# Kernel tuning notes

Measured on AMD Instinct MI355X. Metric: run time of the kernel, lower is better.

The kernel has to match this reference:

```python
import jax, jax.numpy as jnp
import numpy as np

B, TM1, ENC, DEC, OUT = 256, 32, 128, 128, 1


def setup_inputs() -> dict:
    key = jax.random.key(0)
    ks = jax.random.split(key, 16)
    s = 0.05
    inp = {
        "input_encoded": jax.random.normal(ks[0], (B, TM1, ENC), jnp.float32),
        "y_history": jax.random.normal(ks[1], (B, TM1, OUT), jnp.float32),
        # attn_layer: Linear(2*DEC+ENC -> ENC), Tanh, Linear(ENC -> 1)
        "attn_W1": jax.random.normal(ks[2], (ENC, 2 * DEC + ENC), jnp.float32) * s,
        "attn_b1": jnp.zeros((ENC,), jnp.float32),
        "attn_W2": jax.random.normal(ks[3], (1, ENC), jnp.float32) * s,
        "attn_b2": jnp.zeros((1,), jnp.float32),
        # LSTM(input_size=OUT, hidden_size=DEC), pytorch gate order i,f,g,o
        "W_ih": jax.random.normal(ks[4], (4 * DEC, OUT), jnp.float32) * s,
        "W_hh": jax.random.normal(ks[5], (4 * DEC, DEC), jnp.float32) * s,
        "b_ih": jnp.zeros((4 * DEC,), jnp.float32),
        "b_hh": jnp.zeros((4 * DEC,), jnp.float32),
        # fc: Linear(ENC+OUT -> OUT), weight initialized with normal_() in torch
        "fc_W": jax.random.normal(ks[6], (OUT, ENC + OUT), jnp.float32),
        "fc_b": jnp.zeros((OUT,), jnp.float32),
        # fc_final: Linear(DEC+ENC -> OUT)
        "fcf_W": jax.random.normal(ks[7], (OUT, DEC + ENC), jnp.float32) * s,
        "fcf_b": jnp.zeros((OUT,), jnp.float32),
    }
    return inp


def _forward(input_encoded, y_history, attn_W1, attn_b1, attn_W2, attn_b2,
             W_ih, W_hh, b_ih, b_hh, fc_W, fc_b, fcf_W, fcf_b):
    b, tm1, enc = input_encoded.shape
    dec = W_hh.shape[1]

    h0 = jnp.zeros((b, dec), input_encoded.dtype)
    c0 = jnp.zeros((b, dec), input_encoded.dtype)
    ctx0 = jnp.zeros((b, enc), input_encoded.dtype)

    def step(carry, y_t):  # y_t: [B, OUT]
        h, c, _ = carry
        hc = jnp.concatenate([h, c], axis=-1)  # [B, 2*DEC]
        x = jnp.concatenate(
            [jnp.broadcast_to(hc[:, None, :], (b, tm1, 2 * dec)), input_encoded],
            axis=-1)  # [B, T-1, 2*DEC+ENC]
        hdn = jnp.tanh(jnp.einsum('bte,he->bth', x, attn_W1) + attn_b1)
        logits = jnp.einsum('bth,oh->bto', hdn, attn_W2)[..., 0] + attn_b2[0]  # [B, T-1]
        attn = jax.nn.softmax(logits, axis=1)
        ctx = jnp.einsum('bt,bte->be', attn, input_encoded)  # [B, ENC]
        y_tilde = jnp.concatenate([ctx, y_t], axis=1) @ fc_W.T + fc_b  # [B, OUT]
        gates = y_tilde @ W_ih.T + b_ih + h @ W_hh.T + b_hh  # [B, 4*DEC]
        i, f, g, o = jnp.split(gates, 4, axis=-1)
        c_new = jax.nn.sigmoid(f) * c + jax.nn.sigmoid(i) * jnp.tanh(g)
        h_new = jax.nn.sigmoid(o) * jnp.tanh(c_new)
        return (h_new, c_new, ctx), None

    (h, c, ctx), _ = jax.lax.scan(step, (h0, c0, ctx0),
                                  jnp.swapaxes(y_history, 0, 1))
    out = jnp.concatenate([h, ctx], axis=1) @ fcf_W.T + fcf_b + y_history[:, -1]
    return out  # [B, OUT]


def reference(input_encoded, y_history, attn_W1, attn_b1, attn_W2, attn_b2,
              W_ih, W_hh, b_ih, b_hh, fc_W, fc_b, fcf_W, fcf_b):
    return _forward(input_encoded, y_history, attn_W1, attn_b1, attn_W2, attn_b2,
                    W_ih, W_hh, b_ih, b_hh, fc_W, fc_b, fcf_W, fcf_b)
```

## Files before the change

### kernel.cpp

```cpp
#include <hip/hip_runtime.h>


#define TT 32

typedef _Float16 h2_t __attribute__((ext_vector_type(2)));
typedef _Float16 h4_t __attribute__((ext_vector_type(4)));
typedef _Float16 h8_t __attribute__((ext_vector_type(8)));

#if __has_builtin(__builtin_amdgcn_fdot2)
#define FDOT2(a, b, c) __builtin_amdgcn_fdot2((a), (b), (c), false)
#else
static __device__ __forceinline__ float FDOT2(h2_t a, h2_t b, float c) {
    return c + (float)a[0] * (float)b[0] + (float)a[1] * (float)b[1];
}
#endif

__device__ __forceinline__ float dot_h8(h8_t w, h8_t v, float acc) {
    acc = FDOT2(__builtin_shufflevector(w, w, 0, 1), __builtin_shufflevector(v, v, 0, 1), acc);
    acc = FDOT2(__builtin_shufflevector(w, w, 2, 3), __builtin_shufflevector(v, v, 2, 3), acc);
    acc = FDOT2(__builtin_shufflevector(w, w, 4, 5), __builtin_shufflevector(v, v, 4, 5), acc);
    acc = FDOT2(__builtin_shufflevector(w, w, 6, 7), __builtin_shufflevector(v, v, 6, 7), acc);
    return acc;
}
__device__ __forceinline__ h8_t pk8(float4 a, float4 b) {
    h8_t r;
    r[0] = (_Float16)a.x; r[1] = (_Float16)a.y; r[2] = (_Float16)a.z; r[3] = (_Float16)a.w;
    r[4] = (_Float16)b.x; r[5] = (_Float16)b.y; r[6] = (_Float16)b.z; r[7] = (_Float16)b.w;
    return r;
}
__device__ __forceinline__ float fast_tanh(float x) {
    float e = __expf(2.f * x);
    return 1.f - __fdividef(2.f, e + 1.f);
}
__device__ __forceinline__ float fast_sig(float x) {
    return __fdividef(1.f, 1.f + __expf(-x));
}

__global__ __launch_bounds__(512, 2) void decoder_kernel(
    const float* __restrict__ enc_g,
    const float* __restrict__ yh_g,
    const float* __restrict__ W1,
    const float* __restrict__ b1,
    const float* __restrict__ W2,
    const float* __restrict__ b2,
    const float* __restrict__ Wih,
    const float* __restrict__ Whh,
    const float* __restrict__ bih,
    const float* __restrict__ bhh,
    const float* __restrict__ fcW,
    const float* __restrict__ fcB,
    const float* __restrict__ fcfW,
    const float* __restrict__ fcfB,
    float* __restrict__ out)
{
    __shared__ __align__(16) h8_t s_w1a8[512 * 8];
    __shared__ __align__(16) _Float16 s_enc16[TT * 136];
    __shared__ __align__(16) _Float16 s_epre16[TT * 128];
    __shared__ __align__(16) _Float16 s_hc[2 * 272];
    __shared__ __align__(16) _Float16 s_A16[128];
    __shared__ __align__(16) _Float16 s_w216[128];
    __shared__ __align__(16) float s_act[512];
    __shared__ float s_logit[TT];
    __shared__ float s_q[TT];
    __shared__ float s_att[TT];
    __shared__ float s_yh[TT];
    __shared__ float s_ctx[128];

    const int tid = threadIdx.x;
    const int b = blockIdx.x;
    const int lane = tid & 63;
    const int g1 = tid >> 2, s4 = tid & 3;
    const int rx7 = tid & 7;

    {
        const float4* encp = (const float4*)(enc_g + (size_t)b * TT * 128);
#pragma unroll
        for (int r = 0; r < 2; r++) {
            int gi = tid * 2 + r;
            float4 v = encp[gi];
            int t = gi >> 5, e4 = gi & 31;
            h4_t hv;
            hv[0] = (_Float16)v.x; hv[1] = (_Float16)v.y;
            hv[2] = (_Float16)v.z; hv[3] = (_Float16)v.w;
            *(h4_t*)(s_enc16 + t * 136 + e4 * 4) = hv;
        }
    }
    if (tid < 272) ((unsigned int*)s_hc)[tid] = 0u;
    if (tid < 128) s_w216[tid] = (_Float16)W2[tid];
    if (tid < TT) s_yh[tid] = yh_g[b * TT + tid];

    h8_t whhreg[16];
    {
        const float4* wp = (const float4*)(Whh + (size_t)tid * 128);
#pragma unroll
        for (int k = 0; k < 16; k++) whhreg[k] = pk8(wp[2 * k], wp[2 * k + 1]);
    }
    const float wih_r = Wih[tid];
    const float bias_r = bih[tid] + bhh[tid];

    {
        const float4* p = (const float4*)(W1 + g1 * 384 + s4 * 64);
#pragma unroll
        for (int k = 0; k < 8; k++)
            s_w1a8[tid * 8 + (k ^ rx7)] = pk8(p[2 * k], p[2 * k + 1]);
    }
    const float b2v = b2[0];
    const float fcw128 = fcW[128];
    const float fcbv = fcB[0];
    const float fcfbv = fcfB[0];
    __syncthreads();

    {
        const float4* wp = (const float4*)(W1 + g1 * 384 + 256 + s4 * 32);
        h8_t wa = pk8(wp[0], wp[1]), wb = pk8(wp[2], wp[3]);
        h8_t wc = pk8(wp[4], wp[5]), wd = pk8(wp[6], wp[7]);
        const float b1v = b1[g1];
        for (int t = 0; t < TT; t++) {
            const h8_t* ep8 = (const h8_t*)(s_enc16 + t * 136);
            float pa = dot_h8(wa, ep8[s4 * 4 + 0], 0.f);
            float pb = dot_h8(wb, ep8[s4 * 4 + 1], 0.f);
            pa = dot_h8(wc, ep8[s4 * 4 + 2], pa);
            pb = dot_h8(wd, ep8[s4 * 4 + 3], pb);
            float pp = pa + pb;
            pp += __shfl_xor(pp, 1);
            pp += __shfl_xor(pp, 2);
            if (s4 == 0) s_epre16[t * 128 + g1] = (_Float16)(pp + b1v);
        }
    }
    if (tid < 128) {
        const int tq = tid >> 2, sq = tid & 3;
        const float4* fp = (const float4*)(fcW + sq * 32);
        h8_t fa = pk8(fp[0], fp[1]), fb = pk8(fp[2], fp[3]);
        h8_t fc2 = pk8(fp[4], fp[5]), fd = pk8(fp[6], fp[7]);
        const h8_t* ep8 = (const h8_t*)(s_enc16 + tq * 136);
        float pa = dot_h8(fa, ep8[sq * 4 + 0], 0.f);
        float pb = dot_h8(fb, ep8[sq * 4 + 1], 0.f);
        pa = dot_h8(fc2, ep8[sq * 4 + 2], pa);
        pb = dot_h8(fd, ep8[sq * 4 + 3], pb);
        float pq = pa + pb;
        pq += __shfl_xor(pq, 1);
        pq += __shfl_xor(pq, 2);
        if (sq == 0) s_q[tq] = pq;
    }
    float c_reg = 0.f;
    __syncthreads();

    for (int t = 0; t < TT; t++) {
        float gdot;
        {
            const h8_t* hp = (const h8_t*)s_hc;
            float a0 = 0.f, a1 = 0.f, a2 = 0.f, a3 = 0.f;
#pragma unroll
            for (int k = 0; k < 2; k++) {
                a0 = dot_h8(whhreg[4 * k + 0], hp[4 * k + 0], a0);
                a1 = dot_h8(whhreg[4 * k + 1], hp[4 * k + 1], a1);
                a2 = dot_h8(whhreg[4 * k + 2], hp[4 * k + 2], a2);
                a3 = dot_h8(whhreg[4 * k + 3], hp[4 * k + 3], a3);
            }
            __builtin_amdgcn_sched_barrier(0);
#pragma unroll
            for (int k = 2; k < 4; k++) {
                a0 = dot_h8(whhreg[4 * k + 0], hp[4 * k + 0], a0);
                a1 = dot_h8(whhreg[4 * k + 1], hp[4 * k + 1], a1);
                a2 = dot_h8(whhreg[4 * k + 2], hp[4 * k + 2], a2);
                a3 = dot_h8(whhreg[4 * k + 3], hp[4 * k + 3], a3);
            }
            gdot = (a0 + a1) + (a2 + a3) + bias_r;
        }
        __builtin_amdgcn_sched_barrier(0);
        {
            const h8_t* hcp = (const h8_t*)(s_hc + (s4 >> 1) * 272);
            const h8_t* wp8 = s_w1a8 + tid * 8;
            float a0 = 0.f, a1 = 0.f;
#pragma unroll
            for (int k = 0; k < 4; k++) {
                a0 = dot_h8(wp8[(2 * k) ^ rx7], hcp[s4 * 8 + 2 * k], a0);
                a1 = dot_h8(wp8[(2 * k + 1) ^ rx7], hcp[s4 * 8 + 2 * k + 1], a1);
            }
            float aa = a0 + a1;
            aa += __shfl_xor(aa, 1);
            aa += __shfl_xor(aa, 2);
            if (s4 == 0) s_A16[g1] = (_Float16)aa;
        }
        __syncthreads();

        {
            const int tt_ = tid >> 4, sub = tid & 15;
            h8_t ev = ((const h8_t*)(s_epre16 + tt_ * 128))[sub];
            h8_t av = ((const h8_t*)s_A16)[sub];
            h8_t wv = ((const h8_t*)s_w216)[sub];
            float lp = 0.f;
#pragma unroll
            for (int i = 0; i < 8; i++)
                lp += (float)wv[i] * fast_tanh((float)av[i] + (float)ev[i]);
            lp += __shfl_xor(lp, 1);
            lp += __shfl_xor(lp, 2);
            lp += __shfl_xor(lp, 4);
            lp += __shfl_xor(lp, 8);
            if (sub == 0) s_logit[tt_] = lp + b2v;
        }
        __syncthreads();

        float act;
        {
            float el = __expf(s_logit[lane & 31]);
            float ql = s_q[lane & 31];
            float ss = el, ys = el * ql;
#pragma unroll
            for (int m = 1; m <= 16; m <<= 1) {
                ss += __shfl_xor(ss, m);
                ys += __shfl_xor(ys, m);
            }
            float inv = __fdividef(1.f, ss);
            if (t == TT - 1 && tid < TT) s_att[tid] = el * inv;
            float yt = ys * inv + fcw128 * s_yh[t] + fcbv;
            float gv = gdot + wih_r * yt;
            act = ((tid >> 7) == 2) ? fast_tanh(gv) : fast_sig(gv);
            s_act[tid] = act;
        }
        __syncthreads();

        if (tid < 128) {
            float af = s_act[128 + tid];
            float ag = s_act[256 + tid];
            float ao = s_act[384 + tid];
            float cn = af * c_reg + act * ag;
            float hn = ao * fast_tanh(cn);
            c_reg = cn;
            _Float16 hh = (_Float16)hn, cc = (_Float16)cn;
            s_hc[tid] = hh;
            s_hc[128 + tid] = cc;
            s_hc[272 + tid] = hh;
            s_hc[400 + tid] = cc;
        }
        __syncthreads();
    }

    if (tid < 128) {
        float acc = 0.f;
#pragma unroll 8
        for (int t2 = 0; t2 < TT; t2++) acc += s_att[t2] * (float)s_enc16[t2 * 136 + tid];
        s_ctx[tid] = acc;
    }
    __syncthreads();
    if (tid < 64) {
        float p = fcfW[lane] * (float)s_hc[lane] +
                  fcfW[64 + lane] * (float)s_hc[64 + lane] +
                  fcfW[128 + lane] * s_ctx[lane] +
                  fcfW[192 + lane] * s_ctx[64 + lane];
#pragma unroll
        for (int m = 1; m < 64; m <<= 1) p += __shfl_xor(p, m);
        if (lane == 0) out[b] = p + fcfbv + s_yh[TT - 1];
    }
}

extern "C" void kernel_launch(void* const* d_in, const int* in_sizes, int n_in,
                              void* d_out, int out_size, void* d_ws, size_t ws_size,
                              hipStream_t stream) {
    decoder_kernel<<<256, 512, 0, stream>>>(
        (const float*)d_in[0], (const float*)d_in[1], (const float*)d_in[2],
        (const float*)d_in[3], (const float*)d_in[4], (const float*)d_in[5],
        (const float*)d_in[6], (const float*)d_in[7], (const float*)d_in[8],
        (const float*)d_in[9], (const float*)d_in[10], (const float*)d_in[11],
        (const float*)d_in[12], (const float*)d_in[13], (float*)d_out);
}
```

Measured before the change: 173.6 us.

## Keep attention W1 slice in registers and drop one barrier per LSTM step

The per-thread slice of attention W1 (the h,c part) now lives in registers instead of a swizzled LDS array, and its dot product is interleaved with the W_hh recurrent dot product in a single loop. The gate stage is restructured: threads 128-511 write their raw pre-activation gate dots to LDS, and the first 128 threads apply all four gate nonlinearities and the cell update themselves. This removes the s_act round trip and one __syncthreads per timestep, and frees LDS. The cost is more live VGPRs under launch_bounds(512,2), which risks spills or lower occupancy, and 384 threads now sit idle during the gate math.

After: 166.0 us. -4.4%, faster.

```diff
diff --git a/kernel.cpp b/kernel.cpp
--- a/kernel.cpp
+++ b/kernel.cpp
@@ -53,13 +53,12 @@
     const float* __restrict__ fcfB,
     float* __restrict__ out)
 {
-    __shared__ __align__(16) h8_t s_w1a8[512 * 8];
     __shared__ __align__(16) _Float16 s_enc16[TT * 136];
     __shared__ __align__(16) _Float16 s_epre16[TT * 128];
     __shared__ __align__(16) _Float16 s_hc[2 * 272];
     __shared__ __align__(16) _Float16 s_A16[128];
     __shared__ __align__(16) _Float16 s_w216[128];
-    __shared__ __align__(16) float s_act[512];
+    __shared__ __align__(16) float s_gdot3[384];
     __shared__ float s_logit[TT];
     __shared__ float s_q[TT];
     __shared__ float s_att[TT];
@@ -70,7 +69,6 @@
     const int b = blockIdx.x;
     const int lane = tid & 63;
     const int g1 = tid >> 2, s4 = tid & 3;
-    const int rx7 = tid & 7;
 
     {
         const float4* encp = (const float4*)(enc_g + (size_t)b * TT * 128);
@@ -95,14 +93,21 @@
 #pragma unroll
         for (int k = 0; k < 16; k++) whhreg[k] = pk8(wp[2 * k], wp[2 * k + 1]);
     }
-    const float wih_r = Wih[tid];
     const float bias_r = bih[tid] + bhh[tid];
 
+    h8_t w1areg[8];
     {
         const float4* p = (const float4*)(W1 + g1 * 384 + s4 * 64);
 #pragma unroll
-        for (int k = 0; k < 8; k++)
-            s_w1a8[tid * 8 + (k ^ rx7)] = pk8(p[2 * k], p[2 * k + 1]);
+        for (int k = 0; k < 8; k++) w1areg[k] = pk8(p[2 * k], p[2 * k + 1]);
+    }
+
+    float wih0 = 0.f, wih1 = 0.f, wih2 = 0.f, wih3 = 0.f;
+    if (tid < 128) {
+        wih0 = Wih[tid];
+        wih1 = Wih[128 + tid];
+        wih2 = Wih[256 + tid];
+        wih3 = Wih[384 + tid];
     }
     const float b2v = b2[0];
     const float fcw128 = fcW[128];
@@ -146,42 +151,28 @@
     __syncthreads();
 
     for (int t = 0; t < TT; t++) {
-        float gdot;
+        float gdot, aa;
         {
-            const h8_t* hp = (const h8_t*)s_hc;
-            float a0 = 0.f, a1 = 0.f, a2 = 0.f, a3 = 0.f;
-#pragma unroll
-            for (int k = 0; k < 2; k++) {
-                a0 = dot_h8(whhreg[4 * k + 0], hp[4 * k + 0], a0);
-                a1 = dot_h8(whhreg[4 * k + 1], hp[4 * k + 1], a1);
-                a2 = dot_h8(whhreg[4 * k + 2], hp[4 * k + 2], a2);
-                a3 = dot_h8(whhreg[4 * k + 3], hp[4 * k + 3], a3);
+            const h8_t* hp0 = (const h8_t*)s_hc;
+            const h8_t* hpA = (const h8_t*)(s_hc + (s4 & 1) * 272);
+            float a0 = 0.f, a1 = 0.f;
+            float g0 = 0.f, g1v = 0.f, g2 = 0.f, g3 = 0.f;
+#pragma unroll
+            for (int k = 0; k < 4; k++) {
+                a0 = dot_h8(w1areg[2 * k], hpA[s4 * 8 + 2 * k], a0);
+                a1 = dot_h8(w1areg[2 * k + 1], hpA[s4 * 8 + 2 * k + 1], a1);
+                g0 = dot_h8(whhreg[4 * k + 0], hp0[4 * k + 0], g0);
+                g1v = dot_h8(whhreg[4 * k + 1], hp0[4 * k + 1], g1v);
+                g2 = dot_h8(whhreg[4 * k + 2], hp0[4 * k + 2], g2);
+                g3 = dot_h8(whhreg[4 * k + 3], hp0[4 * k + 3], g3);
             }
-            __builtin_amdgcn_sched_barrier(0);
-#pragma unroll
-            for (int k = 2; k < 4; k++) {
-                a0 = dot_h8(whhreg[4 * k + 0], hp[4 * k + 0], a0);
-                a1 = dot_h8(whhreg[4 * k + 1], hp[4 * k + 1], a1);
-                a2 = dot_h8(whhreg[4 * k + 2], hp[4 * k + 2], a2);
-                a3 = dot_h8(whhreg[4 * k + 3], hp[4 * k + 3], a3);
-            }
-            gdot = (a0 + a1) + (a2 + a3) + bias_r;
-        }
-        __builtin_amdgcn_sched_barrier(0);
-        {
-            const h8_t* hcp = (const h8_t*)(s_hc + (s4 >> 1) * 272);
-            const h8_t* wp8 = s_w1a8 + tid * 8;
-            float a0 = 0.f, a1 = 0.f;
-#pragma unroll
-            for (int k = 0; k < 4; k++) {
-                a0 = dot_h8(wp8[(2 * k) ^ rx7], hcp[s4 * 8 + 2 * k], a0);
-                a1 = dot_h8(wp8[(2 * k + 1) ^ rx7], hcp[s4 * 8 + 2 * k + 1], a1);
-            }
-            float aa = a0 + a1;
+            gdot = (g0 + g1v) + (g2 + g3) + bias_r;
+            aa = a0 + a1;
             aa += __shfl_xor(aa, 1);
             aa += __shfl_xor(aa, 2);
-            if (s4 == 0) s_A16[g1] = (_Float16)aa;
-        }
+        }
+        if (s4 == 0) s_A16[g1] = (_Float16)aa;
+        if (tid >= 128) s_gdot3[tid - 128] = gdot;
         __syncthreads();
 
         {
@@ -201,8 +192,7 @@
         }
         __syncthreads();
 
-        float act;
-        {
+        if (tid < 128) {
             float el = __expf(s_logit[lane & 31]);
             float ql = s_q[lane & 31];
             float ss = el, ys = el * ql;
@@ -214,18 +204,12 @@
             float inv = __fdividef(1.f, ss);
             if (t == TT - 1 && tid < TT) s_att[tid] = el * inv;
             float yt = ys * inv + fcw128 * s_yh[t] + fcbv;
-            float gv = gdot + wih_r * yt;
-            act = ((tid >> 7) == 2) ? fast_tanh(gv) : fast_sig(gv);
-            s_act[tid] = act;
-        }
-        __syncthreads();
-
-        if (tid < 128) {
-            float af = s_act[128 + tid];
-            float ag = s_act[256 + tid];
-            float ao = s_act[384 + tid];
-            float cn = af * c_reg + act * ag;
-            float hn = ao * fast_tanh(cn);
+            float gi_ = gdot + wih0 * yt;
+            float gf_ = s_gdot3[tid] + wih1 * yt;
+            float gg_ = s_gdot3[128 + tid] + wih2 * yt;
+            float go_ = s_gdot3[256 + tid] + wih3 * yt;
+            float cn = fast_sig(gf_) * c_reg + fast_sig(gi_) * fast_tanh(gg_);
+            float hn = fast_sig(go_) * fast_tanh(cn);
             c_reg = cn;
             _Float16 hh = (_Float16)hn, cc = (_Float16)cn;
             s_hc[tid] = hh;
```
